# Kernel tuning notes

Hardware: AMD Instinct MI355X
Metric: run time of the kernel (lower is better)

## Reference

```python
import jax, jax.numpy as jnp
import numpy as np

THRESHOLD = 0.5
SLACK = 3
EPS = 1e-12
B, H, W = 16, 512, 512


def _shift(p, dy, dx, b, h, w):
    # p is zero-padded by 1 on spatial dims; returns neighbor at offset (dy, dx)
    return p[:, 1 + dy:1 + dy + h, 1 + dx:1 + dx + w]


def _thin_sub(img, step):
    # One Zhang-Suen sub-iteration on bool image [B,H,W] (zero boundary, as skimage)
    b, h, w = img.shape
    p = jnp.pad(img.astype(jnp.int32), ((0, 0), (1, 1), (1, 1)))
    # P2..P9 clockwise starting at North
    P2 = _shift(p, -1, 0, b, h, w); P3 = _shift(p, -1, 1, b, h, w)
    P4 = _shift(p, 0, 1, b, h, w);  P5 = _shift(p, 1, 1, b, h, w)
    P6 = _shift(p, 1, 0, b, h, w);  P7 = _shift(p, 1, -1, b, h, w)
    P8 = _shift(p, 0, -1, b, h, w); P9 = _shift(p, -1, -1, b, h, w)
    seq = [P2, P3, P4, P5, P6, P7, P8, P9, P2]
    Bn = P2 + P3 + P4 + P5 + P6 + P7 + P8 + P9          # neighbor count
    A = sum((1 - seq[k]) * seq[k + 1] for k in range(8))  # 0->1 transitions
    cond = (Bn >= 2) & (Bn <= 6) & (A == 1)
    if step == 0:
        cond = cond & (P2 * P4 * P6 == 0) & (P4 * P6 * P8 == 0)
    else:
        cond = cond & (P2 * P4 * P8 == 0) & (P2 * P6 * P8 == 0)
    return img & ~cond


def _skeletonize(img):
    # Iterate Zhang-Suen thinning to convergence (skimage.morphology.skeletonize 2D = Zhang's method)
    def body(state):
        cur, _ = state
        nxt = _thin_sub(_thin_sub(cur, 0), 1)
        return (nxt, jnp.any(nxt != cur))

    out, _ = jax.lax.while_loop(lambda s: s[1], body, (img, jnp.array(True)))
    return out


def _edt_sq(mask):
    # Exact squared Euclidean distance to nearest True pixel, separable 2-pass.
    b, h, w = mask.shape
    BIG = h + w  # larger than any attainable 1D distance
    g = jnp.where(mask, 0, BIG).astype(jnp.int32)  # [B,H,W]

    # pass 1: 1D nearest-True distance along rows (axis=1) via fwd/bwd scans
    def fscan(carry, row):
        d = jnp.minimum(row, carry + 1)
        return d, d

    g_rows = jnp.moveaxis(g, 1, 0)  # [H,B,W]
    init = jnp.full((b, w), BIG, jnp.int32)
    _, fwd = jax.lax.scan(fscan, init, g_rows)
    _, bwd = jax.lax.scan(fscan, init, g_rows[::-1])
    f = jnp.minimum(jnp.minimum(fwd, bwd[::-1]), BIG)  # [H,B,W]
    f2 = jnp.moveaxis(f * f, 0, 1)  # [B,H,W] squared vertical distance

    # pass 2: d2[b,i,j] = min_{j'} f2[b,i,j'] + (j-j')^2 (lower envelope, memory-friendly lax.map)
    js = jnp.arange(w, dtype=jnp.int32)

    def one_col(j):
        off = (js - j) ** 2  # [W]
        return jnp.min(f2 + off[None, None, :], axis=-1)  # [B,H]

    d2 = jax.lax.map(one_col, js)  # [W,B,H]
    return jnp.transpose(d2, (1, 2, 0))  # [B,H,W]


def setup_inputs() -> dict:
    key = jax.random.key(0)
    k1, k2 = jax.random.split(key)
    y_pred = jax.random.uniform(k1, (B, H, W), dtype=jnp.float32)
    y_true = jax.random.uniform(k2, (B, H, W), dtype=jnp.float32)
    return {"y_pred": y_pred, "y_true": y_true}


def reference(y_pred, y_true):
    p = y_pred > THRESHOLD  # greater_is_road=True binarization
    g = y_true > THRESHOLD
    p = _skeletonize(p)
    g = _skeletonize(g)
    d2_gt = _edt_sq(g)   # EDT of ~g == distance to nearest g pixel
    d2_pr = _edt_sq(p)
    s2 = SLACK * SLACK   # dist <= slack  <=>  dist^2 <= slack^2 (integer sq EDT)
    tp_area = d2_gt <= s2
    fp_area = ~tp_area
    fn_area = d2_pr > s2
    ax = (1, 2)
    TP = jnp.sum(tp_area & p, ax).astype(jnp.float32)
    FP = jnp.sum(fp_area & p, ax).astype(jnp.float32)
    FN = jnp.sum(fn_area & g, ax).astype(jnp.float32)
    correctness = TP / (TP + FP + EPS)
    completeness = TP / (TP + FN + EPS)
    quality = TP / (TP + FP + FN + EPS)
    # mean over batch -> [3]: [correctness, completeness, quality]
    return jnp.mean(jnp.stack([correctness, completeness, quality], axis=1), axis=0)
```

## Files before the change

kernel.cpp:

```cpp
#include <hip/hip_runtime.h>
#include <stdint.h>

#define HH 512
#define WW 512
#define WPR 8
#define NWORDS (HH * WPR)
#define NTHREADS 1024
#define WPT (NWORDS / NTHREADS)
#define NB 16
#define NMASK (2 * NB)

typedef unsigned long long u64;

__device__ __forceinline__ u64 ldw(const u64* M, int r, int c) {
    return (r < 0 || r >= HH || c < 0 || c >= WPR) ? 0ULL : M[r * WPR + c];
}

__device__ __forceinline__ u64 zs_word(const u64* M, int r, int c, int step) {
    u64 nm = ldw(M, r - 1, c - 1), nc = ldw(M, r - 1, c), np = ldw(M, r - 1, c + 1);
    u64 cm = ldw(M, r,     c - 1), cc = ldw(M, r,     c), cp = ldw(M, r,     c + 1);
    u64 sm = ldw(M, r + 1, c - 1), sc = ldw(M, r + 1, c), sp = ldw(M, r + 1, c + 1);

    u64 P2 = nc;
    u64 P3 = (nc >> 1) | (np << 63);
    u64 P4 = (cc >> 1) | (cp << 63);
    u64 P5 = (sc >> 1) | (sp << 63);
    u64 P6 = sc;
    u64 P7 = (sc << 1) | (sm >> 63);
    u64 P8 = (cc << 1) | (cm >> 63);
    u64 P9 = (nc << 1) | (nm >> 63);

    u64 ab = P2 ^ P3;
    u64 s1 = ab ^ P4, c1 = (P2 & P3) | (ab & P4);
    u64 de = P5 ^ P6;
    u64 s2 = de ^ P7, c2 = (P5 & P6) | (de & P7);
    u64 s3 = P8 ^ P9, c3 = P8 & P9;
    u64 gh = s1 ^ s2;
    u64 b0 = gh ^ s3, c4 = (s1 & s2) | (gh & s3);
    u64 ij = c1 ^ c2;
    u64 s4 = ij ^ c3, c5 = (c1 & c2) | (ij & c3);
    u64 b1 = s4 ^ c4, c6 = s4 & c4;
    u64 b2 = c5 ^ c6, b3 = c5 & c6;

    u64 Bge2 = b1 | b2 | b3;
    u64 Ble6 = ~(b3 | (b2 & b1 & b0));

    u64 a1, a2, t;
    t = ~P2 & P3; a1 = t; a2 = 0ULL;
    t = ~P3 & P4; a2 |= a1 & t; a1 |= t;
    t = ~P4 & P5; a2 |= a1 & t; a1 |= t;
    t = ~P5 & P6; a2 |= a1 & t; a1 |= t;
    t = ~P6 & P7; a2 |= a1 & t; a1 |= t;
    t = ~P7 & P8; a2 |= a1 & t; a1 |= t;
    t = ~P8 & P9; a2 |= a1 & t; a1 |= t;
    t = ~P9 & P2; a2 |= a1 & t; a1 |= t;
    u64 Aeq1 = a1 & ~a2;

    u64 sccond;
    if (step == 0) sccond = ~(P2 & P4 & P6) & ~(P4 & P6 & P8);
    else           sccond = ~(P2 & P4 & P8) & ~(P2 & P6 & P8);

    return cc & ~(Bge2 & Ble6 & Aeq1 & sccond);
}

__device__ __forceinline__ u64 spread4(u64 x) {
    x &= 0xFFFFULL;
    x = (x | (x << 24)) & 0x000000FF000000FFULL;
    x = (x | (x << 12)) & 0x000F000F000F000FULL;
    x = (x | (x << 6))  & 0x0303030303030303ULL;
    x = (x | (x << 3))  & 0x1111111111111111ULL;
    return x;
}

__global__ __launch_bounds__(256)
void pack_kernel(const float* __restrict__ y_pred,
                 const float* __restrict__ y_true,
                 u64* __restrict__ bits ,
                 int* __restrict__ cnt ) {
    if (blockIdx.x == 0 && threadIdx.x < 4 * NB + 1) cnt[threadIdx.x] = 0;
    int wid = (blockIdx.x * 256 + threadIdx.x) >> 6;
    int lane = threadIdx.x & 63;
    int w = lane & 3;
    int sh = w * 16;
    #pragma unroll
    for (int it = 0; it < 4; ++it) {
        int ch = wid * 4 + it;
        int f4 = ch * 64 + lane;
        int img = f4 >> 16;
        const float* src = (img < NB) ? y_pred + (size_t)img * (HH * WW)
                                      : y_true + (size_t)(img - NB) * (HH * WW);
        float4 a = ((const float4*)src)[f4 & 65535];
        u64 B0 = __ballot(a.x > 0.5f);
        u64 B1 = __ballot(a.y > 0.5f);
        u64 B2 = __ballot(a.z > 0.5f);
        u64 B3 = __ballot(a.w > 0.5f);
        u64 word = spread4(B0 >> sh)
                 | (spread4(B1 >> sh) << 1)
                 | (spread4(B2 >> sh) << 2)
                 | (spread4(B3 >> sh) << 3);
        if (lane < 4) bits[ch * 4 + w] = word;
    }
}

__global__ __launch_bounds__(NTHREADS)
void skel_kernel(u64* __restrict__ bits ) {
    __shared__ u64 M[NWORDS];
    __shared__ unsigned int Cp[HH + 2];
    __shared__ int s_any[2];

    int bx = blockIdx.x;
    int tid = threadIdx.x;
    int lane = tid & 63;
    u64* mine = bits + (size_t)bx * NWORDS;

    #pragma unroll
    for (int k = 0; k < WPT; ++k) {
        int wi = k * NTHREADS + tid;
        M[wi] = mine[wi];
    }

    for (int i = tid; i < HH + 2; i += NTHREADS)
        Cp[i] = (i >= 1 && i <= HH) ? 0x1FEu : 0u;
    if (tid < 2) s_any[tid] = 0;

    unsigned dl[WPT];
    #pragma unroll
    for (int k = 0; k < WPT; ++k) dl[k] = 0x1FEu;

    int p = 0;
    for (;;) {
        for (int step = 0; step < 2; ++step) {
            __syncthreads();
            u64 nv[WPT];
            u64 bal[WPT];
            bool anyc = false;
            #pragma unroll
            for (int k = 0; k < WPT; ++k) {
                int wi = k * NTHREADS + tid;
                int r = wi >> 3, c = wi & 7;
                unsigned need = ((Cp[r] | Cp[r + 1] | Cp[r + 2]) >> c) & 7u;
                bool chg = false;
                u64 x = 0;
                if (need) {
                    u64 cur = M[wi];
                    x = zs_word(M, r, c, step);
                    chg = (x != cur);
                }
                nv[k] = x;
                bal[k] = __ballot(chg);
                anyc |= (bal[k] != 0);
            }
            __syncthreads();
            #pragma unroll
            for (int k = 0; k < WPT; ++k) {
                int wi = k * NTHREADS + tid;
                if ((bal[k] >> lane) & 1) M[wi] = nv[k];
                if ((lane & 7) == 0) {
                    unsigned byte = ((unsigned)(bal[k] >> lane) & 0xFFu) << 1;
                    int idx = (wi >> 3) + 1;
                    Cp[idx] = byte | dl[k];
                    dl[k] = byte;
                }
            }
            if (anyc) s_any[p] = 1;
        }
        __syncthreads();
        int done = (s_any[p] == 0);
        if (tid == 0) s_any[p ^ 1] = 0;
        p ^= 1;
        if (done) break;
    }

    #pragma unroll
    for (int k = 0; k < WPT; ++k) {
        int wi = k * NTHREADS + tid;
        mine[wi] = M[wi];
    }
}

#define STRIPS 16
#define SROWS (HH / STRIPS)
#define SR2 (SROWS + 6)
#define CBLOCKS (NB * STRIPS)

__device__ __forceinline__ u64 ldws(const u64* M, int r, int c) {
    return (c < 0 || c >= WPR) ? 0ULL : M[r * WPR + c];
}

__device__ __forceinline__ u64 dil3s(const u64* M, int r, int c) {
    u64 cm = ldws(M, r, c - 1), cc = ldws(M, r, c), cp = ldws(M, r, c + 1);
    u64 h = cc
          | (cc >> 1) | (cp << 63)
          | (cc >> 2) | (cp << 62)
          | (cc >> 3) | (cp << 61)
          | (cc << 1) | (cm >> 63)
          | (cc << 2) | (cm >> 62)
          | (cc << 3) | (cm >> 61);
    u64 um = ldws(M, r - 1, c - 1) | ldws(M, r + 1, c - 1) | ldws(M, r - 2, c - 1) | ldws(M, r + 2, c - 1);
    u64 uc = ldws(M, r - 1, c    ) | ldws(M, r + 1, c    ) | ldws(M, r - 2, c    ) | ldws(M, r + 2, c    );
    u64 up = ldws(M, r - 1, c + 1) | ldws(M, r + 1, c + 1) | ldws(M, r - 2, c + 1) | ldws(M, r + 2, c + 1);
    h |= uc
       | (uc >> 1) | (up << 63)
       | (uc >> 2) | (up << 62)
       | (uc << 1) | (um >> 63)
       | (uc << 2) | (um >> 62);
    h |= ldws(M, r - 3, c) | ldws(M, r + 3, c);
    return h;
}

__global__ __launch_bounds__(256)
void count_kernel(const u64* __restrict__ bits, int* __restrict__ cnt,
                  float* __restrict__ out) {
    __shared__ u64 P[SR2 * WPR];
    __shared__ u64 G[SR2 * WPR];
    __shared__ int acc[4];
    __shared__ int s_last;
    __shared__ int s_cnt[4 * NB];

    int b = blockIdx.x / STRIPS;
    int s = blockIdx.x % STRIPS;
    int tid = threadIdx.x;
    int r0 = s * SROWS - 3;

    const u64* sp = bits + (size_t)b * NWORDS;
    const u64* sg = bits + (size_t)(NB + b) * NWORDS;
    for (int i = tid; i < SR2 * WPR; i += 256) {
        int gr = r0 + (i >> 3);
        bool in = (gr >= 0 && gr < HH);
        int gi = gr * WPR + (i & 7);
        P[i] = in ? sp[gi] : 0ULL;
        G[i] = in ? sg[gi] : 0ULL;
    }
    if (tid < 4) acc[tid] = 0;
    __syncthreads();

    int r = (tid >> 3) + 3, c = tid & 7;
    u64 pw = P[r * WPR + c], gw = G[r * WPR + c];
    int cp  = __popcll(pw);
    int cg  = __popcll(gw);
    int tp  = __popcll(pw & dil3s(G, r, c));
    int fnh = __popcll(gw & dil3s(P, r, c));

    #pragma unroll
    for (int o = 32; o > 0; o >>= 1) {
        cp  += __shfl_down(cp, o);
        cg  += __shfl_down(cg, o);
        tp  += __shfl_down(tp, o);
        fnh += __shfl_down(fnh, o);
    }
    if ((tid & 63) == 0) {
        atomicAdd(&acc[0], cp);
        atomicAdd(&acc[1], cg);
        atomicAdd(&acc[2], tp);
        atomicAdd(&acc[3], fnh);
    }
    __syncthreads();
    if (tid < 4) atomicAdd(&cnt[b * 4 + tid], acc[tid]);

    __threadfence();
    if (tid == 0) {
        int old = atomicAdd(&cnt[4 * NB], 1);
        s_last = (old == CBLOCKS - 1);
    }
    __syncthreads();
    if (!s_last) return;
    __threadfence();
    if (tid < 4 * NB) s_cnt[tid] = atomicAdd(&cnt[tid], 0);
    __syncthreads();
    if (tid < 3) {
        float sum = 0.0f;
        for (int bb = 0; bb < NB; ++bb) {
            float TP = (float)s_cnt[bb * 4 + 2];
            float FP = (float)(s_cnt[bb * 4 + 0] - s_cnt[bb * 4 + 2]);
            float FN = (float)(s_cnt[bb * 4 + 1] - s_cnt[bb * 4 + 3]);
            float v = (tid == 0) ? TP / (TP + FP + 1e-12f)
                    : (tid == 1) ? TP / (TP + FN + 1e-12f)
                                 : TP / (TP + FP + FN + 1e-12f);
            sum += v;
        }
        out[tid] = sum * (1.0f / NB);
    }
}

extern "C" void kernel_launch(void* const* d_in, const int* in_sizes, int n_in,
                              void* d_out, int out_size, void* d_ws, size_t ws_size,
                              hipStream_t stream) {
    (void)in_sizes; (void)n_in; (void)out_size; (void)ws_size;
    const float* y_pred = (const float*)d_in[0];
    const float* y_true = (const float*)d_in[1];
    float* out = (float*)d_out;

    u64* bits = (u64*)d_ws;
    int* cnt = (int*)((char*)d_ws + (size_t)NMASK * NWORDS * sizeof(u64));

    hipLaunchKernelGGL(pack_kernel, dim3(2048), dim3(256), 0, stream,
                       y_pred, y_true, bits, cnt);
    hipLaunchKernelGGL(skel_kernel, dim3(NMASK), dim3(NTHREADS), 0, stream, bits);
    hipLaunchKernelGGL(count_kernel, dim3(CBLOCKS), dim3(256), 0, stream,
                       bits, cnt, out);
}
```

Before: 133.5 us.

## Split each skeletonization image across four blocks with halo exchange

The skeletonization kernel now uses four cooperating workgroups per mask instead of one. Each workgroup owns a 128-row strip, and neighbouring strips exchange boundary rows through global memory after every sub-iteration. A global atomic barrier keeps the strips in step, and a per-iteration change flag decides convergence. This spreads the serial thinning loop over four times as many CUs, at the cost of a grid-wide spin barrier per sub-step. It also assumes all 128 blocks are co-resident and caps the loop at a fixed iteration count.

```diff
diff --git a/kernel.cpp b/kernel.cpp
--- a/kernel.cpp
+++ b/kernel.cpp
@@ -5,21 +5,30 @@
 #define WW 512
 #define WPR 8
 #define NWORDS (HH * WPR)
-#define NTHREADS 1024
-#define WPT (NWORDS / NTHREADS)
 #define NB 16
 #define NMASK (2 * NB)
 
+#define NP 4
+#define PR (HH / NP)
+#define MAXIT 300
+
+#define SYNC_OFF   (NMASK * NWORDS * 8)
+#define CNT_BASE   0
+#define BAR_BASE   72
+#define CHG_BASE   104
+#define SYNC_INTS  (CHG_BASE + NMASK * MAXIT)
+#define HALO_OFF   (SYNC_OFF + 40960)
+
 typedef unsigned long long u64;
 
-__device__ __forceinline__ u64 ldw(const u64* M, int r, int c) {
-    return (r < 0 || r >= HH || c < 0 || c >= WPR) ? 0ULL : M[r * WPR + c];
-}
-
-__device__ __forceinline__ u64 zs_word(const u64* M, int r, int c, int step) {
-    u64 nm = ldw(M, r - 1, c - 1), nc = ldw(M, r - 1, c), np = ldw(M, r - 1, c + 1);
-    u64 cm = ldw(M, r,     c - 1), cc = ldw(M, r,     c), cp = ldw(M, r,     c + 1);
-    u64 sm = ldw(M, r + 1, c - 1), sc = ldw(M, r + 1, c), sp = ldw(M, r + 1, c + 1);
+__device__ __forceinline__ u64 ldh(const u64* M, int lr, int c) {
+    return (c < 0 || c >= WPR) ? 0ULL : M[lr * WPR + c];
+}
+
+__device__ __forceinline__ u64 zs_word(const u64* M, int lr, int c, int step) {
+    u64 nm = ldh(M, lr - 1, c - 1), nc = ldh(M, lr - 1, c), np = ldh(M, lr - 1, c + 1);
+    u64 cm = ldh(M, lr,     c - 1), cc = ldh(M, lr,     c), cp = ldh(M, lr,     c + 1);
+    u64 sm = ldh(M, lr + 1, c - 1), sc = ldh(M, lr + 1, c), sp = ldh(M, lr + 1, c + 1);
 
     u64 P2 = nc;
     u64 P3 = (nc >> 1) | (np << 63);
@@ -75,10 +84,11 @@
 __global__ __launch_bounds__(256)
 void pack_kernel(const float* __restrict__ y_pred,
                  const float* __restrict__ y_true,
-                 u64* __restrict__ bits ,
-                 int* __restrict__ cnt ) {
-    if (blockIdx.x == 0 && threadIdx.x < 4 * NB + 1) cnt[threadIdx.x] = 0;
-    int wid = (blockIdx.x * 256 + threadIdx.x) >> 6;
+                 u64* __restrict__ bits,
+                 int* __restrict__ sync) {
+    int gid = blockIdx.x * 256 + threadIdx.x;
+    if (gid < SYNC_INTS) sync[gid] = 0;
+    int wid = gid >> 6;
     int lane = threadIdx.x & 63;
     int w = lane & 3;
     int sh = w * 16;
@@ -102,80 +112,97 @@
     }
 }
 
-__global__ __launch_bounds__(NTHREADS)
-void skel_kernel(u64* __restrict__ bits ) {
-    __shared__ u64 M[NWORDS];
-    __shared__ unsigned int Cp[HH + 2];
-    __shared__ int s_any[2];
+__global__ __launch_bounds__(1024)
+void skel_kernel(u64* __restrict__ bits, int* __restrict__ sync,
+                 u64* __restrict__ halo) {
+    __shared__ u64 M[(PR + 2) * WPR];
+    __shared__ unsigned Cp[PR + 4];
+    __shared__ int s_chg;
+    __shared__ int s_bc;
 
     int bx = blockIdx.x;
+    int m = bx >> 2, j = bx & (NP - 1);
     int tid = threadIdx.x;
     int lane = tid & 63;
-    u64* mine = bits + (size_t)bx * NWORDS;
-
-    #pragma unroll
-    for (int k = 0; k < WPT; ++k) {
-        int wi = k * NTHREADS + tid;
-        M[wi] = mine[wi];
-    }
-
-    for (int i = tid; i < HH + 2; i += NTHREADS)
-        Cp[i] = (i >= 1 && i <= HH) ? 0x1FEu : 0u;
-    if (tid < 2) s_any[tid] = 0;
-
-    unsigned dl[WPT];
-    #pragma unroll
-    for (int k = 0; k < WPT; ++k) dl[k] = 0x1FEu;
-
-    int p = 0;
-    for (;;) {
+    u64* mine = bits + (size_t)m * NWORDS;
+    int* bar = sync + BAR_BASE + m;
+    int* chg = sync + CHG_BASE + m * MAXIT;
+
+    for (int i = tid; i < (PR + 2) * WPR; i += 1024) {
+        int gr = PR * j - 1 + (i >> 3);
+        M[i] = (gr >= 0 && gr < HH) ? mine[gr * WPR + (i & 7)] : 0ULL;
+    }
+    if (tid < PR + 4) {
+        unsigned v = 0;
+        if (tid >= 2 && tid <= PR + 1) v = 0x1FEu;
+        if (tid == 1) v = (j > 0) ? 0x1FEu : 0u;
+        if (tid == PR + 2) v = (j < NP - 1) ? 0x1FEu : 0u;
+        Cp[tid] = v;
+    }
+    if (tid == 0) s_chg = 0;
+
+    int lr = (tid >> 3) + 1;
+    int c = tid & 7;
+    int wi = lr * WPR + c;
+    int shl = lane & 56;
+    unsigned dl = 0x1FEu;
+
+    int s = 0;
+    for (int it = 0; it < MAXIT; ++it) {
         for (int step = 0; step < 2; ++step) {
             __syncthreads();
-            u64 nv[WPT];
-            u64 bal[WPT];
-            bool anyc = false;
-            #pragma unroll
-            for (int k = 0; k < WPT; ++k) {
-                int wi = k * NTHREADS + tid;
-                int r = wi >> 3, c = wi & 7;
-                unsigned need = ((Cp[r] | Cp[r + 1] | Cp[r + 2]) >> c) & 7u;
-                bool chg = false;
-                u64 x = 0;
-                if (need) {
-                    u64 cur = M[wi];
-                    x = zs_word(M, r, c, step);
-                    chg = (x != cur);
-                }
-                nv[k] = x;
-                bal[k] = __ballot(chg);
-                anyc |= (bal[k] != 0);
+            unsigned need = ((Cp[lr] | Cp[lr + 1] | Cp[lr + 2]) >> c) & 7u;
+            u64 x = 0; bool ch = false;
+            if (need) {
+                x = zs_word(M, lr, c, step);
+                ch = (x != M[wi]);
+            }
+            u64 bal = __ballot(ch);
+            __syncthreads();
+            if ((bal >> lane) & 1) M[wi] = x;
+            unsigned nb = ((unsigned)((bal >> shl) & 0xFFu)) << 1;
+            if ((lane & 7) == 0) Cp[lr + 1] = nb | dl;
+            dl = nb;
+            if (lane == 0 && bal) atomicOr(&s_chg, 1);
+            s++;
+            int par = s & 1;
+            if (j > 0 && lr == 1)
+                __hip_atomic_store(&halo[(((size_t)par * NMASK + m) * NP + j) * 16 + c],
+                                   x, __ATOMIC_RELAXED, __HIP_MEMORY_SCOPE_AGENT);
+            if (j < NP - 1 && lr == PR)
+                __hip_atomic_store(&halo[(((size_t)par * NMASK + m) * NP + j) * 16 + 8 + c],
+                                   x, __ATOMIC_RELAXED, __HIP_MEMORY_SCOPE_AGENT);
+            __syncthreads();
+            if (tid == 0) {
+                if (step == 1 && s_chg)
+                    __hip_atomic_fetch_or(&chg[it], 1, __ATOMIC_RELAXED,
+                                          __HIP_MEMORY_SCOPE_AGENT);
+                __hip_atomic_fetch_add(bar, 1, __ATOMIC_RELEASE,
+                                       __HIP_MEMORY_SCOPE_AGENT);
+                while (__hip_atomic_load(bar, __ATOMIC_ACQUIRE,
+                                         __HIP_MEMORY_SCOPE_AGENT) < NP * s)
+                    __builtin_amdgcn_s_sleep(1);
             }
             __syncthreads();
-            #pragma unroll
-            for (int k = 0; k < WPT; ++k) {
-                int wi = k * NTHREADS + tid;
-                if ((bal[k] >> lane) & 1) M[wi] = nv[k];
-                if ((lane & 7) == 0) {
-                    unsigned byte = ((unsigned)(bal[k] >> lane) & 0xFFu) << 1;
-                    int idx = (wi >> 3) + 1;
-                    Cp[idx] = byte | dl[k];
-                    dl[k] = byte;
-                }
-            }
-            if (anyc) s_any[p] = 1;
+            if (j > 0 && tid < 8)
+                M[tid] = __hip_atomic_load(
+                    &halo[(((size_t)par * NMASK + m) * NP + (j - 1)) * 16 + 8 + tid],
+                    __ATOMIC_RELAXED, __HIP_MEMORY_SCOPE_AGENT);
+            if (j < NP - 1 && tid >= 8 && tid < 16)
+                M[(PR + 1) * WPR + (tid - 8)] = __hip_atomic_load(
+                    &halo[(((size_t)par * NMASK + m) * NP + (j + 1)) * 16 + (tid - 8)],
+                    __ATOMIC_RELAXED, __HIP_MEMORY_SCOPE_AGENT);
+        }
+        if (tid == 0) {
+            s_bc = __hip_atomic_load(&chg[it], __ATOMIC_RELAXED,
+                                     __HIP_MEMORY_SCOPE_AGENT);
+            s_chg = 0;
         }
         __syncthreads();
-        int done = (s_any[p] == 0);
-        if (tid == 0) s_any[p ^ 1] = 0;
-        p ^= 1;
-        if (done) break;
-    }
-
-    #pragma unroll
-    for (int k = 0; k < WPT; ++k) {
-        int wi = k * NTHREADS + tid;
-        mine[wi] = M[wi];
-    }
+        if (s_bc == 0) break;
+    }
+
+    mine[j * (PR * WPR) + tid] = M[wi];
 }
 
 #define STRIPS 16
@@ -183,12 +210,8 @@
 #define SR2 (SROWS + 6)
 #define CBLOCKS (NB * STRIPS)
 
-__device__ __forceinline__ u64 ldws(const u64* M, int r, int c) {
-    return (c < 0 || c >= WPR) ? 0ULL : M[r * WPR + c];
-}
-
 __device__ __forceinline__ u64 dil3s(const u64* M, int r, int c) {
-    u64 cm = ldws(M, r, c - 1), cc = ldws(M, r, c), cp = ldws(M, r, c + 1);
+    u64 cm = ldh(M, r, c - 1), cc = ldh(M, r, c), cp = ldh(M, r, c + 1);
     u64 h = cc
           | (cc >> 1) | (cp << 63)
           | (cc >> 2) | (cp << 62)
@@ -196,15 +219,15 @@
           | (cc << 1) | (cm >> 63)
           | (cc << 2) | (cm >> 62)
           | (cc << 3) | (cm >> 61);
-    u64 um = ldws(M, r - 1, c - 1) | ldws(M, r + 1, c - 1) | ldws(M, r - 2, c - 1) | ldws(M, r + 2, c - 1);
-    u64 uc = ldws(M, r - 1, c    ) | ldws(M, r + 1, c    ) | ldws(M, r - 2, c    ) | ldws(M, r + 2, c    );
-    u64 up = ldws(M, r - 1, c + 1) | ldws(M, r + 1, c + 1) | ldws(M, r - 2, c + 1) | ldws(M, r + 2, c + 1);
+    u64 um = ldh(M, r - 1, c - 1) | ldh(M, r + 1, c - 1) | ldh(M, r - 2, c - 1) | ldh(M, r + 2, c - 1);
+    u64 uc = ldh(M, r - 1, c    ) | ldh(M, r + 1, c    ) | ldh(M, r - 2, c    ) | ldh(M, r + 2, c    );
+    u64 up = ldh(M, r - 1, c + 1) | ldh(M, r + 1, c + 1) | ldh(M, r - 2, c + 1) | ldh(M, r + 2, c + 1);
     h |= uc
        | (uc >> 1) | (up << 63)
        | (uc >> 2) | (up << 62)
        | (uc << 1) | (um >> 63)
        | (uc << 2) | (um >> 62);
-    h |= ldws(M, r - 3, c) | ldws(M, r + 3, c);
+    h |= ldh(M, r - 3, c) | ldh(M, r + 3, c);
     return h;
 }
 
@@ -291,11 +314,13 @@
     float* out = (float*)d_out;
 
     u64* bits = (u64*)d_ws;
-    int* cnt = (int*)((char*)d_ws + (size_t)NMASK * NWORDS * sizeof(u64));
+    int* sync = (int*)((char*)d_ws + SYNC_OFF);
+    u64* halo = (u64*)((char*)d_ws + HALO_OFF);
 
     hipLaunchKernelGGL(pack_kernel, dim3(2048), dim3(256), 0, stream,
-                       y_pred, y_true, bits, cnt);
-    hipLaunchKernelGGL(skel_kernel, dim3(NMASK), dim3(NTHREADS), 0, stream, bits);
+                       y_pred, y_true, bits, sync);
+    hipLaunchKernelGGL(skel_kernel, dim3(NMASK * NP), dim3(1024), 0, stream,
+                       bits, sync, halo);
     hipLaunchKernelGGL(count_kernel, dim3(CBLOCKS), dim3(256), 0, stream,
-                       bits, cnt, out);
-}
+                       bits, sync + CNT_BASE, out);
+}
```

Result: slower. 152.9 us (+14.5%).
